# Kernel tuning notes

Hardware: AMD Instinct MI355X
Metric: run time of the kernel (lower is better)

The kernel has to match this reference:

```python
import jax, jax.numpy as jnp
import numpy as np

N = 8  # fixed node count per sample (hardcoded in the torch module)


def setup_inputs() -> dict:
    key = jax.random.key(0)
    ks = jax.random.split(key, 13)
    B = 131072

    def w(k, shape, fan_in):
        # torch nn.Linear default init: U(-1/sqrt(fan_in), 1/sqrt(fan_in))
        return jax.random.uniform(k, shape, jnp.float32, -1.0, 1.0) / np.sqrt(fan_in).astype(np.float32)

    return {
        "x": jax.random.normal(ks[0], (B, N), jnp.float32),
        "enc_w1": w(ks[1], (3, 64), 3),   "enc_b1": w(ks[2], (64,), 3),
        "enc_w2": w(ks[3], (64, 2), 64),  "enc_b2": w(ks[4], (2,), 64),
        "gcn1_w": w(ks[5], (2, 32), 2),   "gcn1_b": w(ks[6], (32,), 2),
        "gcn2_w": w(ks[7], (32, 32), 32), "gcn2_b": w(ks[8], (32,), 32),
        "dec_w1": w(ks[9], (32, 64), 32), "dec_b1": w(ks[10], (64,), 32),
        "dec_w2": w(ks[11], (64, 3), 64), "dec_b2": w(ks[12], (3,), 64),
    }


def _gabriel_norm_adj(p):
    """Batched Gabriel graph -> GCN-normalized (A + I) with unit edge weights.

    p: (B, N, 2) latent 2D points.
    Edge (i,j) exists iff no other point k lies strictly inside the circle
    with diameter (p_i, p_j)  (dist(p_k, mid)^2 < r^2, matching torch's '<').
    Gabriel graphs contain the nearest-neighbor graph, so for N>=2 edges always
    exist and the torch fallback branch is unreachable.
    Returns D^{-1/2} (A + I) D^{-1/2} of shape (B, N, N) (GCNConv default:
    add_self_loops=True with weight 1, symmetric normalization).
    """
    mid = (p[:, :, None, :] + p[:, None, :, :]) * 0.5                 # (B,N,N,2)
    r2 = jnp.sum((p[:, :, None, :] - mid) ** 2, axis=-1)              # (B,N,N)
    # d2[b,i,j,k] = ||p[b,k] - mid[b,i,j]||^2  -> (B,N,N,N), the big intermediate
    d2 = jnp.sum((p[:, None, None, :, :] - mid[:, :, :, None, :]) ** 2, axis=-1)
    a = jnp.arange(N)
    k_not_ij = (a[None, None, :] != a[:, None, None]) & (a[None, None, :] != a[None, :, None])  # (N,N,N) [i,j,k]
    blocked = jnp.any((d2 < r2[..., None]) & k_not_ij, axis=-1)       # (B,N,N)
    off_diag = a[:, None] != a[None, :]
    adj = ((~blocked) & off_diag).astype(p.dtype)                     # symmetric Gabriel adjacency
    a_hat = adj + jnp.eye(N, dtype=p.dtype)                           # self-loops, weight 1
    dinv = jax.lax.rsqrt(jnp.sum(a_hat, axis=-1))                     # (B,N)
    return dinv[:, :, None] * a_hat * dinv[:, None, :]


def reference(x, enc_w1, enc_b1, enc_w2, enc_b2,
              gcn1_w, gcn1_b, gcn2_w, gcn2_b,
              dec_w1, dec_b1, dec_w2, dec_b2):
    B = x.shape[0]
    idx = jnp.arange(N, dtype=x.dtype)
    # preprocess: (B, N, 3) rows [0, value, index]
    xp = jnp.stack([jnp.zeros_like(x), x, jnp.broadcast_to(idx, x.shape)], axis=-1)
    latent = jax.nn.relu(xp @ enc_w1 + enc_b1) @ enc_w2 + enc_b2      # (B,N,2)
    # torch builds the graph from detach().cpu().numpy() -> no grad through structure
    norm = jax.lax.stop_gradient(_gabriel_norm_adj(latent))           # (B,N,N)
    h1 = jax.nn.relu(jnp.einsum('bij,bjf->bif', norm, latent @ gcn1_w) + gcn1_b)  # (B,N,32)
    h2 = jnp.einsum('bij,bjf->bif', norm, h1 @ gcn2_w) + gcn2_b                    # (B,N,32)
    pooled = jnp.mean(h2, axis=1)                                     # (B,32)
    node = jnp.broadcast_to(pooled[:, None, :], (B, N, pooled.shape[-1]))
    dec = jax.nn.relu(node @ dec_w1 + dec_b1) @ dec_w2 + dec_b2       # (B,N,3)
    reconstructed = dec[:, :, 1]                                      # (B,N)
    return reconstructed, latent
```

## Files before the change

kernel.cpp:

```cpp
#include <hip/hip_runtime.h>


typedef float v2 __attribute__((ext_vector_type(2)));

static __device__ __forceinline__ v2 sp(float s) { return (v2){s, s}; }
static __device__ __forceinline__ v2 fma2(v2 a, v2 b, v2 c) {
    return __builtin_elementwise_fma(a, b, c);
}
static __device__ __forceinline__ v2 ldv2(const float* p) {
    return *reinterpret_cast<const v2*>(p);
}

__global__ __launch_bounds__(256, 2) void gae_kernel(
    const float* __restrict__ x,
    const float* __restrict__ enc_w1,
    const float* __restrict__ enc_b1,
    const float* __restrict__ enc_w2,
    const float* __restrict__ enc_b2,
    const float* __restrict__ gcn1_w,
    const float* __restrict__ gcn1_b,
    const float* __restrict__ gcn2_w,
    const float* __restrict__ gcn2_b,
    const float* __restrict__ dec_w1,
    const float* __restrict__ dec_b1,
    const float* __restrict__ dec_w2,
    const float* __restrict__ dec_b2,
    float* __restrict__ out_rec,
    float* __restrict__ out_lat,
    int B)
{
    const int b = blockIdx.x * blockDim.x + threadIdx.x;
    if (b >= B) return;

    float xv[8];
    {
        const float4* xp = reinterpret_cast<const float4*>(x + (size_t)b * 8);
        float4 a = xp[0], c = xp[1];
        xv[0] = a.x; xv[1] = a.y; xv[2] = a.z; xv[3] = a.w;
        xv[4] = c.x; xv[5] = c.y; xv[6] = c.z; xv[7] = c.w;
    }
    v2 xv2[4];
    #pragma unroll
    for (int ip = 0; ip < 4; ++ip) xv2[ip] = (v2){xv[2 * ip], xv[2 * ip + 1]};

    v2 p[8];
    {
        const v2 b2v = ldv2(enc_b2);
        #pragma unroll
        for (int i = 0; i < 8; ++i) p[i] = b2v;
    }
    #pragma unroll 4
    for (int h = 0; h < 64; ++h) {
        const float wx = enc_w1[64 + h];
        const float wi = enc_w1[128 + h];
        const float bb = enc_b1[h];
        const v2 uxy = ldv2(enc_w2 + 2 * h);
        #pragma unroll
        for (int ip = 0; ip < 4; ++ip) {
            v2 c2 = fma2((v2){(float)(2 * ip), (float)(2 * ip + 1)}, sp(wi), sp(bb));
            v2 t2 = fma2(xv2[ip], sp(wx), c2);
            float t0 = fmaxf(t2.x, 0.0f);
            float t1 = fmaxf(t2.y, 0.0f);
            p[2 * ip]     = fma2(sp(t0), uxy, p[2 * ip]);
            p[2 * ip + 1] = fma2(sp(t1), uxy, p[2 * ip + 1]);
        }
    }

    {
        float4* lo = reinterpret_cast<float4*>(out_lat + (size_t)b * 16);
        lo[0] = make_float4(p[0].x, p[0].y, p[1].x, p[1].y);
        lo[1] = make_float4(p[2].x, p[2].y, p[3].x, p[3].y);
        lo[2] = make_float4(p[4].x, p[4].y, p[5].x, p[5].y);
        lo[3] = make_float4(p[6].x, p[6].y, p[7].x, p[7].y);
    }

    float af[8][8];
    #pragma unroll
    for (int i = 0; i < 8; ++i)
        #pragma unroll
        for (int j = 0; j < 8; ++j) af[i][j] = (i == j) ? 1.0f : 0.0f;
    {
        #pragma clang fp contract(off)
        #pragma unroll
        for (int i = 0; i < 8; ++i) {
            #pragma unroll
            for (int j = i + 1; j < 8; ++j) {
                v2 mid = (p[i] + p[j]) * sp(0.5f);
                v2 di = p[i] - mid;  v2 si = di * di;  float r2i = si.x + si.y;
                v2 dj = p[j] - mid;  v2 sj = dj * dj;  float r2j = sj.x + sj.y;
                float dmin = 3.4e38f;
                #pragma unroll
                for (int k = 0; k < 8; ++k) {
                    if (k == i || k == j) continue;
                    v2 dk = p[k] - mid;
                    v2 sk = dk * dk;
                    dmin = fminf(dmin, sk.x + sk.y);
                }
                af[i][j] = (dmin < r2i) ? 0.0f : 1.0f;
                af[j][i] = (dmin < r2j) ? 0.0f : 1.0f;
            }
        }
    }

    float dinv[8];
    #pragma unroll
    for (int i = 0; i < 8; ++i) {
        float s = ((af[i][0] + af[i][1]) + (af[i][2] + af[i][3])) +
                  ((af[i][4] + af[i][5]) + (af[i][6] + af[i][7]));
        dinv[i] = __builtin_amdgcn_rsqf(s);
    }

    v2 q[8];
    #pragma unroll
    for (int j = 0; j < 8; ++j) q[j] = sp(dinv[j]) * p[j];

    v2 n[8];
    #pragma unroll
    for (int i = 0; i < 8; ++i) {
        v2 acc = sp(af[i][0]) * q[0];
        #pragma unroll
        for (int j = 1; j < 8; ++j) acc = fma2(sp(af[i][j]), q[j], acc);
        n[i] = sp(dinv[i]) * acc;
    }

    float cj[8];
    #pragma unroll
    for (int jp = 0; jp < 4; ++jp) {
        v2 acc = (v2){af[0][2 * jp], af[0][2 * jp + 1]} * sp(dinv[0]);
        #pragma unroll
        for (int i = 1; i < 8; ++i)
            acc = fma2((v2){af[i][2 * jp], af[i][2 * jp + 1]}, sp(dinv[i]), acc);
        v2 c2 = (sp(0.125f) * (v2){dinv[2 * jp], dinv[2 * jp + 1]}) * acc;
        cj[2 * jp] = c2.x; cj[2 * jp + 1] = c2.y;
    }

    v2 t2[16];
    #pragma unroll
    for (int fp = 0; fp < 16; ++fp) t2[fp] = sp(0.0f);
    #pragma unroll
    for (int i = 0; i < 8; ++i) {
        const v2 nxi = sp(n[i].x), nyi = sp(n[i].y), ci = sp(cj[i]);
        #pragma unroll
        for (int fp = 0; fp < 16; ++fp) {
            v2 h = fma2(nxi, ldv2(gcn1_w + 2 * fp),
                   fma2(nyi, ldv2(gcn1_w + 32 + 2 * fp), ldv2(gcn1_b + 2 * fp)));
            h = __builtin_elementwise_max(h, sp(0.0f));
            t2[fp] = fma2(ci, h, t2[fp]);
        }
    }

    v2 pooled2[16];
    #pragma unroll
    for (int gp = 0; gp < 16; ++gp) pooled2[gp] = ldv2(gcn2_b + 2 * gp);
    #pragma unroll
    for (int f = 0; f < 32; ++f) {
        const v2 tf = sp(t2[f >> 1][f & 1]);
        #pragma unroll
        for (int gp = 0; gp < 16; ++gp)
            pooled2[gp] = fma2(tf, ldv2(gcn2_w + f * 32 + 2 * gp), pooled2[gp]);
    }

    v2 a2[32];
    #pragma unroll
    for (int hp = 0; hp < 32; ++hp) a2[hp] = ldv2(dec_b1 + 2 * hp);
    #pragma unroll
    for (int f = 0; f < 32; ++f) {
        const v2 pf = sp(pooled2[f >> 1][f & 1]);
        #pragma unroll
        for (int hp = 0; hp < 32; ++hp)
            a2[hp] = fma2(pf, ldv2(dec_w1 + f * 64 + 2 * hp), a2[hp]);
    }
    float o0 = 0.0f, o1 = 0.0f;
    #pragma unroll
    for (int hp = 0; hp < 32; ++hp) {
        v2 r = __builtin_elementwise_max(a2[hp], sp(0.0f));
        o0 = fmaf(r.x, dec_w2[(2 * hp) * 3 + 1], o0);
        o1 = fmaf(r.y, dec_w2[(2 * hp + 1) * 3 + 1], o1);
    }
    const float outv = (o0 + o1) + dec_b2[1];

    {
        float4 r4 = make_float4(outv, outv, outv, outv);
        float4* ro = reinterpret_cast<float4*>(out_rec + (size_t)b * 8);
        ro[0] = r4;
        ro[1] = r4;
    }
}

extern "C" void kernel_launch(void* const* d_in, const int* in_sizes, int n_in,
                              void* d_out, int out_size, void* d_ws, size_t ws_size,
                              hipStream_t stream) {
    const float* x       = (const float*)d_in[0];
    const float* enc_w1  = (const float*)d_in[1];
    const float* enc_b1  = (const float*)d_in[2];
    const float* enc_w2  = (const float*)d_in[3];
    const float* enc_b2  = (const float*)d_in[4];
    const float* gcn1_w  = (const float*)d_in[5];
    const float* gcn1_b  = (const float*)d_in[6];
    const float* gcn2_w  = (const float*)d_in[7];
    const float* gcn2_b  = (const float*)d_in[8];
    const float* dec_w1  = (const float*)d_in[9];
    const float* dec_b1  = (const float*)d_in[10];
    const float* dec_w2  = (const float*)d_in[11];
    const float* dec_b2  = (const float*)d_in[12];

    const int B = in_sizes[0] / 8;
    float* out_rec = (float*)d_out;
    float* out_lat = out_rec + (size_t)B * 8;

    const int threads = 256;
    const int blocks  = (B + threads - 1) / threads;
    gae_kernel<<<blocks, threads, 0, stream>>>(
        x, enc_w1, enc_b1, enc_w2, enc_b2,
        gcn1_w, gcn1_b, gcn2_w, gcn2_b,
        dec_w1, dec_b1, dec_w2, dec_b2,
        out_rec, out_lat, B);
}
```

Measured before the change: 120.5 us.

## Fold gcn2 into decoder weights and split each sample across two wavefronts

```diff
diff --git a/kernel.cpp b/kernel.cpp
--- a/kernel.cpp
+++ b/kernel.cpp
@@ -2,7 +2,6 @@
 
 
 typedef float v2 __attribute__((ext_vector_type(2)));
-
 static __device__ __forceinline__ v2 sp(float s) { return (v2){s, s}; }
 static __device__ __forceinline__ v2 fma2(v2 a, v2 b, v2 c) {
     return __builtin_elementwise_fma(a, b, c);
@@ -11,7 +10,29 @@
     return *reinterpret_cast<const v2*>(p);
 }
 
-__global__ __launch_bounds__(256, 2) void gae_kernel(
+__global__ __launch_bounds__(256) void gae_aux(
+    const float* __restrict__ gcn2_w, const float* __restrict__ gcn2_b,
+    const float* __restrict__ dec_w1, const float* __restrict__ dec_b1,
+    const float* __restrict__ dec_w2, float* __restrict__ ws)
+{
+    const int tid = blockIdx.x * 256 + threadIdx.x;
+    const int f = tid >> 6, h = tid & 63;
+    float acc = 0.0f;
+    #pragma unroll 8
+    for (int g = 0; g < 32; ++g)
+        acc = fmaf(gcn2_w[f * 32 + g], dec_w1[g * 64 + h], acc);
+    ws[f * 64 + h] = acc;
+    if (tid < 64) {
+        float c = dec_b1[h];
+        #pragma unroll 8
+        for (int g = 0; g < 32; ++g)
+            c = fmaf(gcn2_b[g], dec_w1[g * 64 + h], c);
+        ws[2048 + h] = c;
+        ws[2112 + h] = dec_w2[h * 3 + 1];
+    }
+}
+
+__global__ __launch_bounds__(256, 4) void gae_main(
     const float* __restrict__ x,
     const float* __restrict__ enc_w1,
     const float* __restrict__ enc_b1,
@@ -19,35 +40,34 @@
     const float* __restrict__ enc_b2,
     const float* __restrict__ gcn1_w,
     const float* __restrict__ gcn1_b,
-    const float* __restrict__ gcn2_w,
-    const float* __restrict__ gcn2_b,
-    const float* __restrict__ dec_w1,
-    const float* __restrict__ dec_b1,
-    const float* __restrict__ dec_w2,
+    const float* __restrict__ ws,
     const float* __restrict__ dec_b2,
     float* __restrict__ out_rec,
     float* __restrict__ out_lat,
     int B)
 {
-    const int b = blockIdx.x * blockDim.x + threadIdx.x;
-    if (b >= B) return;
-
-    float xv[8];
-    {
-        const float4* xp = reinterpret_cast<const float4*>(x + (size_t)b * 8);
-        float4 a = xp[0], c = xp[1];
-        xv[0] = a.x; xv[1] = a.y; xv[2] = a.z; xv[3] = a.w;
-        xv[4] = c.x; xv[5] = c.y; xv[6] = c.z; xv[7] = c.w;
-    }
-    v2 xv2[4];
-    #pragma unroll
-    for (int ip = 0; ip < 4; ++ip) xv2[ip] = (v2){xv[2 * ip], xv[2 * ip + 1]};
-
-    v2 p[8];
+    __shared__ v2    pbuf[2][8][64];
+    __shared__ v2    tbuf[2][16][64];
+    __shared__ float obuf[2][2][64];
+
+    const int lane = threadIdx.x & 63;
+    const int wid  = threadIdx.x >> 6;
+    const int wp   = wid >> 1;
+    const int ru   = __builtin_amdgcn_readfirstlane(wid & 1);
+    int g = blockIdx.x * 128 + wp * 64 + lane;
+    if (g >= B) g = B - 1;
+
+    const float4 xr = *reinterpret_cast<const float4*>(x + (size_t)g * 8 + 4 * ru);
+    const v2 xA = (v2){xr.x, xr.y};
+    const v2 xB = (v2){xr.z, xr.w};
+    const float i0 = (float)(4 * ru);
+    const v2 ipA = (v2){i0, i0 + 1.0f};
+    const v2 ipB = (v2){i0 + 2.0f, i0 + 3.0f};
+
+    v2 pl0, pl1, pl2, pl3;
     {
         const v2 b2v = ldv2(enc_b2);
-        #pragma unroll
-        for (int i = 0; i < 8; ++i) p[i] = b2v;
+        pl0 = b2v; pl1 = b2v; pl2 = b2v; pl3 = b2v;
     }
     #pragma unroll 4
     for (int h = 0; h < 64; ++h) {
@@ -55,30 +75,36 @@
         const float wi = enc_w1[128 + h];
         const float bb = enc_b1[h];
         const v2 uxy = ldv2(enc_w2 + 2 * h);
-        #pragma unroll
-        for (int ip = 0; ip < 4; ++ip) {
-            v2 c2 = fma2((v2){(float)(2 * ip), (float)(2 * ip + 1)}, sp(wi), sp(bb));
-            v2 t2 = fma2(xv2[ip], sp(wx), c2);
-            float t0 = fmaxf(t2.x, 0.0f);
-            float t1 = fmaxf(t2.y, 0.0f);
-            p[2 * ip]     = fma2(sp(t0), uxy, p[2 * ip]);
-            p[2 * ip + 1] = fma2(sp(t1), uxy, p[2 * ip + 1]);
-        }
-    }
-
-    {
-        float4* lo = reinterpret_cast<float4*>(out_lat + (size_t)b * 16);
-        lo[0] = make_float4(p[0].x, p[0].y, p[1].x, p[1].y);
-        lo[1] = make_float4(p[2].x, p[2].y, p[3].x, p[3].y);
-        lo[2] = make_float4(p[4].x, p[4].y, p[5].x, p[5].y);
-        lo[3] = make_float4(p[6].x, p[6].y, p[7].x, p[7].y);
-    }
-
-    float af[8][8];
-    #pragma unroll
-    for (int i = 0; i < 8; ++i)
-        #pragma unroll
-        for (int j = 0; j < 8; ++j) af[i][j] = (i == j) ? 1.0f : 0.0f;
+        v2 cA = fma2(ipA, sp(wi), sp(bb));
+        v2 cB = fma2(ipB, sp(wi), sp(bb));
+        v2 tA = fma2(xA, sp(wx), cA);
+        v2 tB = fma2(xB, sp(wx), cB);
+        tA = __builtin_elementwise_max(tA, sp(0.0f));
+        tB = __builtin_elementwise_max(tB, sp(0.0f));
+        pl0 = fma2(sp(tA.x), uxy, pl0);
+        pl1 = fma2(sp(tA.y), uxy, pl1);
+        pl2 = fma2(sp(tB.x), uxy, pl2);
+        pl3 = fma2(sp(tB.y), uxy, pl3);
+    }
+
+    {
+        float4* lo = reinterpret_cast<float4*>(out_lat + (size_t)g * 16 + 8 * ru);
+        lo[0] = make_float4(pl0.x, pl0.y, pl1.x, pl1.y);
+        lo[1] = make_float4(pl2.x, pl2.y, pl3.x, pl3.y);
+    }
+
+    pbuf[wp][4 * ru + 0][lane] = pl0;
+    pbuf[wp][4 * ru + 1][lane] = pl1;
+    pbuf[wp][4 * ru + 2][lane] = pl2;
+    pbuf[wp][4 * ru + 3][lane] = pl3;
+    __syncthreads();
+    v2 p[8];
+    #pragma unroll
+    for (int j = 0; j < 8; ++j) p[j] = pbuf[wp][j][lane];
+
+    unsigned m[8];
+    #pragma unroll
+    for (int i = 0; i < 8; ++i) m[i] = 1u << i;
     {
         #pragma clang fp contract(off)
         #pragma unroll
@@ -96,94 +122,95 @@
                     v2 sk = dk * dk;
                     dmin = fminf(dmin, sk.x + sk.y);
                 }
-                af[i][j] = (dmin < r2i) ? 0.0f : 1.0f;
-                af[j][i] = (dmin < r2j) ? 0.0f : 1.0f;
+                m[i] |= (dmin < r2i) ? 0u : (1u << j);
+                m[j] |= (dmin < r2j) ? 0u : (1u << i);
             }
         }
     }
 
     float dinv[8];
     #pragma unroll
+    for (int i = 0; i < 8; ++i)
+        dinv[i] = __builtin_amdgcn_rsqf((float)__popc(m[i]));
+
+    v2 q[8];
+    #pragma unroll
+    for (int j = 0; j < 8; ++j) q[j] = sp(dinv[j]) * p[j];
+
+    v2 n[8];
+    #pragma unroll
     for (int i = 0; i < 8; ++i) {
-        float s = ((af[i][0] + af[i][1]) + (af[i][2] + af[i][3])) +
-                  ((af[i][4] + af[i][5]) + (af[i][6] + af[i][7]));
-        dinv[i] = __builtin_amdgcn_rsqf(s);
-    }
-
-    v2 q[8];
-    #pragma unroll
-    for (int j = 0; j < 8; ++j) q[j] = sp(dinv[j]) * p[j];
-
-    v2 n[8];
-    #pragma unroll
-    for (int i = 0; i < 8; ++i) {
-        v2 acc = sp(af[i][0]) * q[0];
-        #pragma unroll
-        for (int j = 1; j < 8; ++j) acc = fma2(sp(af[i][j]), q[j], acc);
+        v2 acc = sp(0.0f);
+        #pragma unroll
+        for (int j = 0; j < 8; ++j)
+            acc = fma2(sp((float)((m[i] >> j) & 1u)), q[j], acc);
         n[i] = sp(dinv[i]) * acc;
     }
 
     float cj[8];
     #pragma unroll
-    for (int jp = 0; jp < 4; ++jp) {
-        v2 acc = (v2){af[0][2 * jp], af[0][2 * jp + 1]} * sp(dinv[0]);
-        #pragma unroll
-        for (int i = 1; i < 8; ++i)
-            acc = fma2((v2){af[i][2 * jp], af[i][2 * jp + 1]}, sp(dinv[i]), acc);
-        v2 c2 = (sp(0.125f) * (v2){dinv[2 * jp], dinv[2 * jp + 1]}) * acc;
-        cj[2 * jp] = c2.x; cj[2 * jp + 1] = c2.y;
-    }
-
-    v2 t2[16];
-    #pragma unroll
-    for (int fp = 0; fp < 16; ++fp) t2[fp] = sp(0.0f);
+    for (int j = 0; j < 8; ++j) {
+        float s = 0.0f;
+        #pragma unroll
+        for (int i = 0; i < 8; ++i)
+            s = fmaf((float)((m[i] >> j) & 1u), dinv[i], s);
+        cj[j] = 0.125f * dinv[j] * s;
+    }
+
+    const float* w0 = gcn1_w + 16 * ru;
+    const float* w1 = gcn1_w + 32 + 16 * ru;
+    const float* bl = gcn1_b + 16 * ru;
+    v2 t2[8];
+    #pragma unroll
+    for (int fp = 0; fp < 8; ++fp) t2[fp] = sp(0.0f);
     #pragma unroll
     for (int i = 0; i < 8; ++i) {
         const v2 nxi = sp(n[i].x), nyi = sp(n[i].y), ci = sp(cj[i]);
         #pragma unroll
-        for (int fp = 0; fp < 16; ++fp) {
-            v2 h = fma2(nxi, ldv2(gcn1_w + 2 * fp),
-                   fma2(nyi, ldv2(gcn1_w + 32 + 2 * fp), ldv2(gcn1_b + 2 * fp)));
+        for (int fp = 0; fp < 8; ++fp) {
+            v2 h = fma2(nxi, ldv2(w0 + 2 * fp),
+                   fma2(nyi, ldv2(w1 + 2 * fp), ldv2(bl + 2 * fp)));
             h = __builtin_elementwise_max(h, sp(0.0f));
             t2[fp] = fma2(ci, h, t2[fp]);
         }
     }
 
-    v2 pooled2[16];
-    #pragma unroll
-    for (int gp = 0; gp < 16; ++gp) pooled2[gp] = ldv2(gcn2_b + 2 * gp);
+    #pragma unroll
+    for (int fp = 0; fp < 8; ++fp) tbuf[wp][8 * ru + fp][lane] = t2[fp];
+    __syncthreads();
+    v2 tf[16];
+    #pragma unroll
+    for (int fp = 0; fp < 16; ++fp) tf[fp] = tbuf[wp][fp][lane];
+
+    const float* Wd = ws + 32 * ru;
+    const float* cd = ws + 2048 + 32 * ru;
+    const float* w2 = ws + 2112 + 32 * ru;
+    v2 a2[16];
+    #pragma unroll
+    for (int hp = 0; hp < 16; ++hp) a2[hp] = ldv2(cd + 2 * hp);
     #pragma unroll
     for (int f = 0; f < 32; ++f) {
-        const v2 tf = sp(t2[f >> 1][f & 1]);
-        #pragma unroll
-        for (int gp = 0; gp < 16; ++gp)
-            pooled2[gp] = fma2(tf, ldv2(gcn2_w + f * 32 + 2 * gp), pooled2[gp]);
-    }
-
-    v2 a2[32];
-    #pragma unroll
-    for (int hp = 0; hp < 32; ++hp) a2[hp] = ldv2(dec_b1 + 2 * hp);
-    #pragma unroll
-    for (int f = 0; f < 32; ++f) {
-        const v2 pf = sp(pooled2[f >> 1][f & 1]);
-        #pragma unroll
-        for (int hp = 0; hp < 32; ++hp)
-            a2[hp] = fma2(pf, ldv2(dec_w1 + f * 64 + 2 * hp), a2[hp]);
-    }
-    float o0 = 0.0f, o1 = 0.0f;
-    #pragma unroll
-    for (int hp = 0; hp < 32; ++hp) {
-        v2 r = __builtin_elementwise_max(a2[hp], sp(0.0f));
-        o0 = fmaf(r.x, dec_w2[(2 * hp) * 3 + 1], o0);
-        o1 = fmaf(r.y, dec_w2[(2 * hp + 1) * 3 + 1], o1);
-    }
-    const float outv = (o0 + o1) + dec_b2[1];
+        const v2 pf = sp(tf[f >> 1][f & 1]);
+        const float* wr = Wd + f * 64;
+        #pragma unroll
+        for (int hp = 0; hp < 16; ++hp)
+            a2[hp] = fma2(pf, ldv2(wr + 2 * hp), a2[hp]);
+    }
+    v2 oacc = sp(0.0f);
+    #pragma unroll
+    for (int hp = 0; hp < 16; ++hp) {
+        v2 rr = __builtin_elementwise_max(a2[hp], sp(0.0f));
+        oacc = fma2(rr, ldv2(w2 + 2 * hp), oacc);
+    }
+    const float opart = oacc.x + oacc.y;
+
+    obuf[wp][ru][lane] = opart;
+    __syncthreads();
+    const float outv = (opart + obuf[wp][1 - ru][lane]) + dec_b2[1];
 
     {
         float4 r4 = make_float4(outv, outv, outv, outv);
-        float4* ro = reinterpret_cast<float4*>(out_rec + (size_t)b * 8);
-        ro[0] = r4;
-        ro[1] = r4;
+        *reinterpret_cast<float4*>(out_rec + (size_t)g * 8 + 4 * ru) = r4;
     }
 }
 
@@ -207,12 +234,14 @@
     const int B = in_sizes[0] / 8;
     float* out_rec = (float*)d_out;
     float* out_lat = out_rec + (size_t)B * 8;
+    float* ws      = (float*)d_ws;
+
+    gae_aux<<<8, 256, 0, stream>>>(gcn2_w, gcn2_b, dec_w1, dec_b1, dec_w2, ws);
 
     const int threads = 256;
-    const int blocks  = (B + threads - 1) / threads;
-    gae_kernel<<<blocks, threads, 0, stream>>>(
+    const int blocks  = (2 * B + threads - 1) / threads;
+    gae_main<<<blocks, threads, 0, stream>>>(
         x, enc_w1, enc_b1, enc_w2, enc_b2,
-        gcn1_w, gcn1_b, gcn2_w, gcn2_b,
-        dec_w1, dec_b1, dec_w2, dec_b2,
+        gcn1_w, gcn1_b, ws, dec_b2,
         out_rec, out_lat, B);
 }
```

New measurement: 113.7 us. 5.6% less time.
